# Kernel optimization log

Hardware: AMD Instinct MI355X
Metric: run time of the kernel (lower is better)

## Reference

```python
import jax, jax.numpy as jnp
import numpy as np

WS = 7        # window_size
SHIFT = 3     # shift_size
NH = 3        # num_heads
E = 96        # embed_dim
B, H, W = 8, 224, 224


def _relative_position_index(ws: int) -> np.ndarray:
    coords = np.stack(np.meshgrid(np.arange(ws), np.arange(ws), indexing='ij')).reshape(2, -1)
    rel = coords[:, :, None] - coords[:, None, :]          # (2, N, N)
    rel = rel.transpose(1, 2, 0) + (ws - 1)                # (N, N, 2)
    rel[:, :, 0] *= 2 * ws - 1
    return rel.sum(-1)                                      # (N, N) in [0, (2ws-1)^2)


def setup_inputs() -> dict:
    key = jax.random.key(0)
    ks = jax.random.split(key, 6)
    x = jax.random.normal(ks[0], (B, H, W, E), dtype=jnp.float32)
    # nn.MultiheadAttention params: packed in_proj (3E,E)+(3E,), out_proj (E,E)+(E,)
    w_qkv = jax.random.normal(ks[1], (3 * E, E), dtype=jnp.float32) * 0.02
    b_qkv = jax.random.normal(ks[2], (3 * E,), dtype=jnp.float32) * 0.02
    w_out = jax.random.normal(ks[3], (E, E), dtype=jnp.float32) * 0.02
    b_out = jax.random.normal(ks[4], (E,), dtype=jnp.float32) * 0.02
    bias_table = jax.random.normal(ks[5], ((2 * WS - 1) ** 2, NH), dtype=jnp.float32) * 0.02
    rel_index = jnp.asarray(_relative_position_index(WS), dtype=jnp.int32)
    return {"x": x, "w_qkv": w_qkv, "b_qkv": b_qkv, "w_out": w_out,
            "b_out": b_out, "bias_table": bias_table, "rel_index": rel_index}


def reference(x, w_qkv, b_qkv, w_out, b_out, bias_table, rel_index):
    ws, shift = WS, SHIFT
    Bq, Hq, Wq, C = x.shape
    nh = bias_table.shape[-1]
    hd = C // nh
    N = ws * ws

    # cyclic shift
    xs = jnp.roll(x, (-shift, -shift), axis=(1, 2))

    Hp = -(-Hq // ws) * ws
    Wp = -(-Wq // ws) * ws
    xs = jnp.pad(xs, ((0, 0), (0, Hp - Hq), (0, Wp - Wq), (0, 0)))

    # window partition -> (B*nW, N, C)
    win = xs.reshape(Bq, Hp // ws, ws, Wp // ws, ws, C)
    win = win.transpose(0, 1, 3, 2, 4, 5).reshape(-1, N, C)

    # packed QKV projection (torch Linear: x @ W.T + b)
    qkv = win @ w_qkv.T + b_qkv
    q, k, v = jnp.split(qkv, 3, axis=-1)
    hsplit = lambda t: t.reshape(t.shape[0], N, nh, hd)
    q, k, v = hsplit(q), hsplit(k), hsplit(v)

    # scaled attention scores + relative position bias (used as attn_mask in torch)
    scale = 1.0 / jnp.sqrt(jnp.asarray(hd, dtype=q.dtype))
    scores = jnp.einsum('bnhd,bmhd->bhnm', q * scale, k)    # (B*nW, h, N, N)
    bias = bias_table[rel_index].transpose(2, 0, 1)         # (h, N, N)
    attn = jax.nn.softmax(scores + bias[None], axis=-1)

    out = jnp.einsum('bhnm,bmhd->bnhd', attn, v).reshape(-1, N, C)
    out = out @ w_out.T + b_out

    # window reverse + crop + reverse shift
    out = out.reshape(Bq, Hp // ws, Wp // ws, ws, ws, C)
    out = out.transpose(0, 1, 3, 2, 4, 5).reshape(Bq, Hp, Wp, C)[:, :Hq, :Wq, :]
    return jnp.roll(out, (shift, shift), axis=(1, 2))
```

## Files before the change

kernel.cpp:

```cpp
#include <hip/hip_runtime.h>
#include <cstddef>


typedef _Float16 half8 __attribute__((ext_vector_type(8)));
typedef float f4v __attribute__((ext_vector_type(4)));
typedef unsigned short u16;
typedef unsigned int u32;

#define MFMA(A, B, C) __builtin_amdgcn_mfma_f32_16x16x32_f16((A), (B), (C), 0, 0, 0)

__device__ inline u16 f16b(float f) { return __builtin_bit_cast(u16, (_Float16)f); }
__device__ inline u32 pkrtz(float a, float b) {
    return __builtin_bit_cast(u32, __builtin_amdgcn_cvt_pkrtz(a, b));
}
__device__ inline int SWU(int a, int kg) {
    return (((a ^ (kg << 1) ^ ((a & 8) >> 1)) & 15) | (kg << 4));
}

__global__ void prep_kernel(const float* __restrict__ wqkv, const float* __restrict__ wout,
                            const float* __restrict__ btab, const int* __restrict__ ridx,
                            const float* __restrict__ bqkv,
                            u16* __restrict__ wq16, u16* __restrict__ wo16,
                            float* __restrict__ bmf, float* __restrict__ bqs)
{
    const int i = blockIdx.x * 256 + threadIdx.x;
    const float LOG2E = 1.4426950408889634f;
    const float QS = 0.17677669529663688f * LOG2E;
    if (i < 27648) {
        float f = wqkv[i];
        if (i < 9216) f *= QS;
        wq16[i] = f16b(f);
    } else if (i < 36864) {
        wo16[i - 27648] = f16b(wout[i - 27648]);
    } else if (i < 49152) {
        const int j  = i - 36864;
        const int fi = j & 3, ln = (j >> 2) & 63, fw = (j >> 8) & 3;
        const int fut = (j >> 10) & 3, fh = j >> 12;
        const int u  = fut * 16 + (ln >> 4) * 4 + fi;
        const int tt = fw * 16 + (ln & 15);
        float v;
        if (u >= 49)      v = -1e30f;
        else if (tt >= 49) v = 0.f;
        else               v = btab[ridx[tt * 49 + u] * 3 + fh] * LOG2E;
        bmf[j] = v;
    } else if (i < 49440) {
        const int j = i - 49152;
        float f = bqkv[j];
        if (j < 96) f *= QS;
        bqs[j] = f;
    }
}

__global__ __launch_bounds__(256, 4)
void swin_kernel(const float* __restrict__ x,
                 const u16* __restrict__ wq16,
                 const u16* __restrict__ wo16,
                 const float* __restrict__ bqs,
                 const float* __restrict__ bout,
                 const float* __restrict__ bmf,
                 float* __restrict__ out)
{
    __shared__ __attribute__((aligned(16))) char smem[40960];
    constexpr int QT = 0, KT = 12288, VT = 24576, PL = 36864;

    const int tid  = threadIdx.x;
    const int w    = tid >> 6;
    const int lane = tid & 63;
    const int l15  = lane & 15;
    const int lg   = lane >> 4;

    const int blk = blockIdx.x;
    const int bb  = blk >> 10;
    const int wi7 = ((blk >> 5) & 31) * 7;
    const int wj7 = (blk & 31) * 7;

    const int swbase = SWU(l15, lg) * 16;
    const int elb    = ((lg & 1) * 4) * 2;

    half8 xb[4][3];
    #pragma unroll
    for (int m = 0; m < 4; ++m) {
        const int t = m * 16 + l15;
        const int tr = t / 7, tc = t - tr * 7;
        int r = wi7 + tr + 3; if (r >= 224) r -= 224;
        int c = wj7 + tc + 3; if (c >= 224) c -= 224;
        const float* xrow = x + ((size_t)((bb * 224 + r) * 224 + c)) * 96 + lg * 8;
        #pragma unroll
        for (int ks = 0; ks < 3; ++ks) {
            const float4 f0 = *(const float4*)(xrow + ks * 32);
            const float4 f1 = *(const float4*)(xrow + ks * 32 + 4);
            uint4 pk;
            pk.x = pkrtz(f0.x, f0.y); pk.y = pkrtz(f0.z, f0.w);
            pk.z = pkrtz(f1.x, f1.y); pk.w = pkrtz(f1.z, f1.w);
            xb[m][ks] = __builtin_bit_cast(half8, pk);
        }
    }
    {
        const u16* wbase = wq16 + (size_t)l15 * 96 + lg * 8;
        half8 bcur[3], bnxt[3];
        int n = w;
        {
            const u16* p = wbase + n * 1536;
            bcur[0] = *(const half8*)(p);
            bcur[1] = *(const half8*)(p + 32);
            bcur[2] = *(const half8*)(p + 64);
        }
        while (true) {
            const int n2 = n + 4;
            if (n2 < 18) {
                const u16* p = wbase + n2 * 1536;
                bnxt[0] = *(const half8*)(p);
                bnxt[1] = *(const half8*)(p + 32);
                bnxt[2] = *(const half8*)(p + 64);
            }
            if (n < 12) {
                const float4 b4 = *(const float4*)(bqs + n * 16 + lg * 4);
                const int kg = ((n & 1) << 1) + (lg >> 1);
                const int fr0 = (n < 6) ? (QT + (((n >> 1) * 4) << 10))
                                        : (KT + ((((n - 6) >> 1) * 4) << 10));
                #pragma unroll
                for (int m = 0; m < 4; ++m) {
                    f4v acc = {0.f, 0.f, 0.f, 0.f};
                    acc = MFMA(bcur[0], xb[m][0], acc);
                    acc = MFMA(bcur[1], xb[m][1], acc);
                    acc = MFMA(bcur[2], xb[m][2], acc);
                    uint2 pv;
                    pv.x = pkrtz(acc[0] + b4.x, acc[1] + b4.y);
                    pv.y = pkrtz(acc[2] + b4.z, acc[3] + b4.w);
                    *(uint2*)(smem + fr0 + (m << 10) + SWU(l15, kg) * 16 + elb) = pv;
                }
            } else {
                const float bv = bqs[n * 16 + l15];
                const int hh = (n - 12) >> 1, nd = n & 1;
                const int fr0 = VT + (((hh * 2 + nd) * 2) << 10);
                #pragma unroll
                for (int m = 0; m < 4; ++m) {
                    f4v acc = {0.f, 0.f, 0.f, 0.f};
                    acc = MFMA(xb[m][0], bcur[0], acc);
                    acc = MFMA(xb[m][1], bcur[1], acc);
                    acc = MFMA(xb[m][2], bcur[2], acc);
                    uint2 pv;
                    pv.x = pkrtz(acc[0] + bv, acc[1] + bv);
                    pv.y = pkrtz(acc[2] + bv, acc[3] + bv);
                    const int kg = ((m & 1) << 1) + (lg >> 1);
                    *(uint2*)(smem + fr0 + ((m >> 1) << 10) + SWU(l15, kg) * 16 + elb) = pv;
                }
            }
            if (n2 >= 18) break;
            bcur[0] = bnxt[0]; bcur[1] = bnxt[1]; bcur[2] = bnxt[2];
            n = n2;
        }
    }
    __syncthreads();

    {
        const int plb = PL + (w << 10);
        half8 qaC, qaN;
        half8 kb[2][4];
        f4v   s[2][4];
        f4v   bC[4];

        qaC = *(const half8*)(smem + QT + ((0 * 4 + w) << 10) + swbase);
        #pragma unroll
        for (int ut = 0; ut < 4; ++ut)
            kb[0][ut] = *(const half8*)(smem + KT + ((0 * 4 + ut) << 10) + swbase);
        {
            const float* bb0 = bmf + w * 256 + lane * 4;
            #pragma unroll
            for (int ut = 0; ut < 4; ++ut) bC[ut] = *(const f4v*)(bb0 + ut * 1024);
        }
        #pragma unroll
        for (int ut = 0; ut < 4; ++ut)
            s[0][ut] = MFMA(kb[0][ut], qaC, bC[ut]);

        #pragma unroll
        for (int h = 0; h < 3; ++h) {
            const int cur = h & 1, nxt = cur ^ 1;
            const int qfr = QT + ((h * 4 + w) << 10);
            if (h < 2) {
                qaN = *(const half8*)(smem + QT + (((h + 1) * 4 + w) << 10) + swbase);
                #pragma unroll
                for (int ut = 0; ut < 4; ++ut)
                    kb[nxt][ut] = *(const half8*)(smem + KT + (((h + 1) * 4 + ut) << 10) + swbase);
                const float* bbn = bmf + (h + 1) * 4096 + w * 256 + lane * 4;
                #pragma unroll
                for (int ut = 0; ut < 4; ++ut) bC[ut] = *(const f4v*)(bbn + ut * 1024);
            }
            float mx = fmaxf(fmaxf(s[cur][0][0], s[cur][0][1]), fmaxf(s[cur][0][2], s[cur][0][3]));
            #pragma unroll
            for (int ut = 1; ut < 4; ++ut) {
                mx = fmaxf(mx, fmaxf(fmaxf(s[cur][ut][0], s[cur][ut][1]),
                                     fmaxf(s[cur][ut][2], s[cur][ut][3])));
            }
            mx = fmaxf(mx, __shfl_xor(mx, 16));
            mx = fmaxf(mx, __shfl_xor(mx, 32));
            float sm = 0.f;
            #pragma unroll
            for (int ut = 0; ut < 4; ++ut)
                #pragma unroll
                for (int i = 0; i < 4; ++i) {
                    const float e = exp2f(s[cur][ut][i] - mx);
                    s[cur][ut][i] = e; sm += e;
                }
            sm += __shfl_xor(sm, 16);
            sm += __shfl_xor(sm, 32);
            const float inv = 1.f / sm;
            #pragma unroll
            for (int ut = 0; ut < 4; ++ut) {
                uint2 pv;
                pv.x = pkrtz(s[cur][ut][0] * inv, s[cur][ut][1] * inv);
                pv.y = pkrtz(s[cur][ut][2] * inv, s[cur][ut][3] * inv);
                const int kg = (ut & 1) * 2 + (lg >> 1);
                const int base = (ut < 2) ? qfr : plb;
                *(uint2*)(smem + base + SWU(l15, kg) * 16 + elb) = pv;
            }
            const half8 vb00 = *(const half8*)(smem + VT + (((h * 2 + 0) * 2 + 0) << 10) + swbase);
            const half8 vb01 = *(const half8*)(smem + VT + (((h * 2 + 0) * 2 + 1) << 10) + swbase);
            const half8 vb10 = *(const half8*)(smem + VT + (((h * 2 + 1) * 2 + 0) << 10) + swbase);
            const half8 vb11 = *(const half8*)(smem + VT + (((h * 2 + 1) * 2 + 1) << 10) + swbase);
            if (h < 2) {
                #pragma unroll
                for (int ut = 0; ut < 4; ++ut)
                    s[nxt][ut] = MFMA(kb[nxt][ut], qaN, bC[ut]);
            }
            const half8 p0 = *(const half8*)(smem + qfr + swbase);
            const half8 p1 = *(const half8*)(smem + plb + swbase);
            #pragma unroll
            for (int nd = 0; nd < 2; ++nd) {
                f4v o = {0.f, 0.f, 0.f, 0.f};
                o = MFMA(nd ? vb10 : vb00, p0, o);
                o = MFMA(nd ? vb11 : vb01, p1, o);
                uint2 ov;
                ov.x = pkrtz(o[0], o[1]);
                ov.y = pkrtz(o[2], o[3]);
                *(uint2*)(smem + qfr + SWU(l15, nd * 2 + (lg >> 1)) * 16 + elb) = ov;
            }
        }
    }

    {
        const half8 ob0 = *(const half8*)(smem + QT + ((0 * 4 + w) << 10) + swbase);
        const half8 ob1 = *(const half8*)(smem + QT + ((1 * 4 + w) << 10) + swbase);
        const half8 ob2 = *(const half8*)(smem + QT + ((2 * 4 + w) << 10) + swbase);
        const int t = w * 16 + l15;
        float* obase = nullptr;
        if (t < 49) {
            const int tr = t / 7, tc = t - tr * 7;
            int r = wi7 + tr + 3; if (r >= 224) r -= 224;
            int c = wj7 + tc + 3; if (c >= 224) c -= 224;
            obase = out + ((size_t)((bb * 224 + r) * 224 + c)) * 96;
        }
        #pragma unroll
        for (int nn = 0; nn < 6; ++nn) {
            const u16* wp = wo16 + (size_t)(nn * 16 + l15) * 96 + lg * 8;
            f4v acc = {0.f, 0.f, 0.f, 0.f};
            acc = MFMA(*(const half8*)(wp),      ob0, acc);
            acc = MFMA(*(const half8*)(wp + 32), ob1, acc);
            acc = MFMA(*(const half8*)(wp + 64), ob2, acc);
            if (obase) {
                const float4 bo = *(const float4*)(bout + nn * 16 + lg * 4);
                float4 res;
                res.x = acc[0] + bo.x; res.y = acc[1] + bo.y;
                res.z = acc[2] + bo.z; res.w = acc[3] + bo.w;
                *(float4*)(obase + nn * 16 + lg * 4) = res;
            }
        }
    }
}

extern "C" void kernel_launch(void* const* d_in, const int* in_sizes, int n_in,
                              void* d_out, int out_size, void* d_ws, size_t ws_size,
                              hipStream_t stream) {
    const float* x          = (const float*)d_in[0];
    const float* w_qkv      = (const float*)d_in[1];
    const float* b_qkv      = (const float*)d_in[2];
    const float* w_out      = (const float*)d_in[3];
    const float* b_out      = (const float*)d_in[4];
    const float* bias_table = (const float*)d_in[5];
    const int*   rel_index  = (const int*)d_in[6];
    float* outp = (float*)d_out;

    u16* wq16 = (u16*)d_ws;
    u16* wo16 = wq16 + 27648;
    float* bmf = (float*)((char*)d_ws + 73728);
    float* bqs = (float*)((char*)d_ws + 122880);

    prep_kernel<<<dim3(194), dim3(256), 0, stream>>>(
        w_qkv, w_out, bias_table, rel_index, b_qkv, wq16, wo16, bmf, bqs);
    swin_kernel<<<dim3(8192), dim3(256), 0, stream>>>(
        x, wq16, wo16, bqs, b_out, bmf, outp);
}
```

Measured before the change: 208.7 us.

## Keep Q and attention output in registers via bpermute, shrink LDS for occupancy

Each wave now computes the Q projection for only its own 16 tokens and keeps the result in registers. A ds_bpermute reshuffle turns it into the MFMA operand layout, so the Q tile never goes through LDS. The attention output is regathered the same way and feeds the output projection straight from registers. LDS shrinks from 40 KB to 32 KB and launch bounds go from 4 to 5 blocks per CU, aiming at higher occupancy. The cost is more cross-lane permute work, the loss of the software pipelining of the next head's score MFMA, and possible register pressure under the tighter bound.

```diff
diff --git a/kernel.cpp b/kernel.cpp
--- a/kernel.cpp
+++ b/kernel.cpp
@@ -8,6 +8,7 @@
 typedef unsigned int u32;
 
 #define MFMA(A, B, C) __builtin_amdgcn_mfma_f32_16x16x32_f16((A), (B), (C), 0, 0, 0)
+#define BPERM(addr, val) __builtin_amdgcn_ds_bpermute((addr), (val))
 
 __device__ inline u16 f16b(float f) { return __builtin_bit_cast(u16, (_Float16)f); }
 __device__ inline u32 pkrtz(float a, float b) {
@@ -39,7 +40,7 @@
         const int u  = fut * 16 + (ln >> 4) * 4 + fi;
         const int tt = fw * 16 + (ln & 15);
         float v;
-        if (u >= 49)      v = -1e30f;
+        if (u >= 49)       v = -1e30f;
         else if (tt >= 49) v = 0.f;
         else               v = btab[ridx[tt * 49 + u] * 3 + fh] * LOG2E;
         bmf[j] = v;
@@ -51,7 +52,7 @@
     }
 }
 
-__global__ __launch_bounds__(256, 4)
+__global__ __launch_bounds__(256, 5)
 void swin_kernel(const float* __restrict__ x,
                  const u16* __restrict__ wq16,
                  const u16* __restrict__ wo16,
@@ -60,8 +61,8 @@
                  const float* __restrict__ bmf,
                  float* __restrict__ out)
 {
-    __shared__ __attribute__((aligned(16))) char smem[40960];
-    constexpr int QT = 0, KT = 12288, VT = 24576, PL = 36864;
+    __shared__ __attribute__((aligned(16))) char smem[32768];
+    constexpr int KT = 0, VT = 12288, PP = 24576;
 
     const int tid  = threadIdx.x;
     const int w    = tid >> 6;
@@ -75,16 +76,16 @@
     const int wj7 = (blk & 31) * 7;
 
     const int swbase = SWU(l15, lg) * 16;
-    const int elb    = ((lg & 1) * 4) * 2;
-
-    half8 xb[4][3];
-    #pragma unroll
-    for (int m = 0; m < 4; ++m) {
-        const int t = m * 16 + l15;
+    const int elb    = (lg & 1) * 8;
+
+    auto pixoff = [&](int t) -> size_t {
         const int tr = t / 7, tc = t - tr * 7;
         int r = wi7 + tr + 3; if (r >= 224) r -= 224;
         int c = wj7 + tc + 3; if (c >= 224) c -= 224;
-        const float* xrow = x + ((size_t)((bb * 224 + r) * 224 + c)) * 96 + lg * 8;
+        return ((size_t)((bb * 224 + r) * 224 + c)) * 96;
+    };
+    auto loadxb = [&](int t, half8* dst) {
+        const float* xrow = x + pixoff(t) + lg * 8;
         #pragma unroll
         for (int ks = 0; ks < 3; ++ks) {
             const float4 f0 = *(const float4*)(xrow + ks * 32);
@@ -92,106 +93,136 @@
             uint4 pk;
             pk.x = pkrtz(f0.x, f0.y); pk.y = pkrtz(f0.z, f0.w);
             pk.z = pkrtz(f1.x, f1.y); pk.w = pkrtz(f1.z, f1.w);
-            xb[m][ks] = __builtin_bit_cast(half8, pk);
-        }
-    }
+            dst[ks] = __builtin_bit_cast(half8, pk);
+        }
+    };
+
+    u32 qd[12];
     {
+        half8 xbw[3];
+        loadxb(w * 16 + l15, xbw);
         const u16* wbase = wq16 + (size_t)l15 * 96 + lg * 8;
         half8 bcur[3], bnxt[3];
-        int n = w;
-        {
-            const u16* p = wbase + n * 1536;
-            bcur[0] = *(const half8*)(p);
-            bcur[1] = *(const half8*)(p + 32);
-            bcur[2] = *(const half8*)(p + 64);
-        }
-        while (true) {
-            const int n2 = n + 4;
-            if (n2 < 18) {
-                const u16* p = wbase + n2 * 1536;
+        bcur[0] = *(const half8*)(wbase);
+        bcur[1] = *(const half8*)(wbase + 32);
+        bcur[2] = *(const half8*)(wbase + 64);
+        #pragma unroll
+        for (int n = 0; n < 6; ++n) {
+            if (n < 5) {
+                const u16* p = wbase + (n + 1) * 1536;
                 bnxt[0] = *(const half8*)(p);
                 bnxt[1] = *(const half8*)(p + 32);
                 bnxt[2] = *(const half8*)(p + 64);
             }
-            if (n < 12) {
-                const float4 b4 = *(const float4*)(bqs + n * 16 + lg * 4);
-                const int kg = ((n & 1) << 1) + (lg >> 1);
-                const int fr0 = (n < 6) ? (QT + (((n >> 1) * 4) << 10))
-                                        : (KT + ((((n - 6) >> 1) * 4) << 10));
-                #pragma unroll
-                for (int m = 0; m < 4; ++m) {
+            f4v acc = {0.f, 0.f, 0.f, 0.f};
+            acc = MFMA(bcur[0], xbw[0], acc);
+            acc = MFMA(bcur[1], xbw[1], acc);
+            acc = MFMA(bcur[2], xbw[2], acc);
+            const float4 b4 = *(const float4*)(bqs + n * 16 + lg * 4);
+            qd[2 * n]     = pkrtz(acc[0] + b4.x, acc[1] + b4.y);
+            qd[2 * n + 1] = pkrtz(acc[2] + b4.z, acc[3] + b4.w);
+            if (n < 5) { bcur[0] = bnxt[0]; bcur[1] = bnxt[1]; bcur[2] = bnxt[2]; }
+        }
+    }
+
+    {
+        half8 kvw[3][3];
+        #pragma unroll
+        for (int i = 0; i < 3; ++i) {
+            const u16* p = wq16 + (size_t)(6 + w + 4 * i) * 1536 + (size_t)l15 * 96 + lg * 8;
+            kvw[i][0] = *(const half8*)(p);
+            kvw[i][1] = *(const half8*)(p + 32);
+            kvw[i][2] = *(const half8*)(p + 64);
+        }
+        half8 xc[3], xn[3];
+        loadxb(l15, xc);
+        #pragma unroll
+        for (int m = 0; m < 4; ++m) {
+            if (m < 3) loadxb((m + 1) * 16 + l15, xn);
+            #pragma unroll
+            for (int i = 0; i < 3; ++i) {
+                const int n = 6 + w + 4 * i;
+                if (n < 12) {
                     f4v acc = {0.f, 0.f, 0.f, 0.f};
-                    acc = MFMA(bcur[0], xb[m][0], acc);
-                    acc = MFMA(bcur[1], xb[m][1], acc);
-                    acc = MFMA(bcur[2], xb[m][2], acc);
+                    acc = MFMA(kvw[i][0], xc[0], acc);
+                    acc = MFMA(kvw[i][1], xc[1], acc);
+                    acc = MFMA(kvw[i][2], xc[2], acc);
+                    const float4 b4 = *(const float4*)(bqs + n * 16 + lg * 4);
                     uint2 pv;
                     pv.x = pkrtz(acc[0] + b4.x, acc[1] + b4.y);
                     pv.y = pkrtz(acc[2] + b4.z, acc[3] + b4.w);
+                    const int kg  = ((n & 1) << 1) + (lg >> 1);
+                    const int fr0 = KT + ((((n - 6) >> 1) * 4) << 10);
                     *(uint2*)(smem + fr0 + (m << 10) + SWU(l15, kg) * 16 + elb) = pv;
-                }
-            } else {
-                const float bv = bqs[n * 16 + l15];
-                const int hh = (n - 12) >> 1, nd = n & 1;
-                const int fr0 = VT + (((hh * 2 + nd) * 2) << 10);
-                #pragma unroll
-                for (int m = 0; m < 4; ++m) {
+                } else {
                     f4v acc = {0.f, 0.f, 0.f, 0.f};
-                    acc = MFMA(xb[m][0], bcur[0], acc);
-                    acc = MFMA(xb[m][1], bcur[1], acc);
-                    acc = MFMA(xb[m][2], bcur[2], acc);
+                    acc = MFMA(xc[0], kvw[i][0], acc);
+                    acc = MFMA(xc[1], kvw[i][1], acc);
+                    acc = MFMA(xc[2], kvw[i][2], acc);
+                    const float bv = bqs[n * 16 + l15];
                     uint2 pv;
                     pv.x = pkrtz(acc[0] + bv, acc[1] + bv);
                     pv.y = pkrtz(acc[2] + bv, acc[3] + bv);
+                    const int hh = (n - 12) >> 1, nd = n & 1;
                     const int kg = ((m & 1) << 1) + (lg >> 1);
-                    *(uint2*)(smem + fr0 + ((m >> 1) << 10) + SWU(l15, kg) * 16 + elb) = pv;
+                    *(uint2*)(smem + VT + ((((hh * 2 + nd) * 2) + (m >> 1)) << 10) +
+                              SWU(l15, kg) * 16 + elb) = pv;
                 }
             }
-            if (n2 >= 18) break;
-            bcur[0] = bnxt[0]; bcur[1] = bnxt[1]; bcur[2] = bnxt[2];
-            n = n2;
-        }
+            if (m < 3) { xc[0] = xn[0]; xc[1] = xn[1]; xc[2] = xn[2]; }
+        }
+    }
+
+    const int sl0 = (l15 + 16 * ((lg & 1) * 2)) << 2;
+    const int sl1 = sl0 + (16 << 2);
+    const bool hi = (lg >= 2);
+    half8 qa[3];
+    #pragma unroll
+    for (int h = 0; h < 3; ++h) {
+        const int A0 = BPERM(sl0, (int)qd[4 * h + 0]), B0 = BPERM(sl0, (int)qd[4 * h + 2]);
+        const int A1 = BPERM(sl0, (int)qd[4 * h + 1]), B1 = BPERM(sl0, (int)qd[4 * h + 3]);
+        const int A2 = BPERM(sl1, (int)qd[4 * h + 0]), B2 = BPERM(sl1, (int)qd[4 * h + 2]);
+        const int A3 = BPERM(sl1, (int)qd[4 * h + 1]), B3 = BPERM(sl1, (int)qd[4 * h + 3]);
+        uint4 qw;
+        qw.x = (u32)(hi ? B0 : A0);
+        qw.y = (u32)(hi ? B1 : A1);
+        qw.z = (u32)(hi ? B2 : A2);
+        qw.w = (u32)(hi ? B3 : A3);
+        qa[h] = __builtin_bit_cast(half8, qw);
     }
     __syncthreads();
 
+    uint4 obw[3];
     {
-        const int plb = PL + (w << 10);
-        half8 qaC, qaN;
-        half8 kb[2][4];
-        f4v   s[2][4];
-        f4v   bC[4];
-
-        qaC = *(const half8*)(smem + QT + ((0 * 4 + w) << 10) + swbase);
+        const int ppb = PP + (w << 11);
+        half8 kb[4]; f4v bC[4];
         #pragma unroll
         for (int ut = 0; ut < 4; ++ut)
-            kb[0][ut] = *(const half8*)(smem + KT + ((0 * 4 + ut) << 10) + swbase);
+            kb[ut] = *(const half8*)(smem + KT + (ut << 10) + swbase);
         {
-            const float* bb0 = bmf + w * 256 + lane * 4;
-            #pragma unroll
-            for (int ut = 0; ut < 4; ++ut) bC[ut] = *(const f4v*)(bb0 + ut * 1024);
-        }
-        #pragma unroll
-        for (int ut = 0; ut < 4; ++ut)
-            s[0][ut] = MFMA(kb[0][ut], qaC, bC[ut]);
-
+            const float* bp = bmf + w * 256 + lane * 4;
+            #pragma unroll
+            for (int ut = 0; ut < 4; ++ut) bC[ut] = *(const f4v*)(bp + ut * 1024);
+        }
         #pragma unroll
         for (int h = 0; h < 3; ++h) {
-            const int cur = h & 1, nxt = cur ^ 1;
-            const int qfr = QT + ((h * 4 + w) << 10);
+            f4v s[4];
+            #pragma unroll
+            for (int ut = 0; ut < 4; ++ut)
+                s[ut] = MFMA(kb[ut], qa[h], bC[ut]);
             if (h < 2) {
-                qaN = *(const half8*)(smem + QT + (((h + 1) * 4 + w) << 10) + swbase);
                 #pragma unroll
                 for (int ut = 0; ut < 4; ++ut)
-                    kb[nxt][ut] = *(const half8*)(smem + KT + (((h + 1) * 4 + ut) << 10) + swbase);
-                const float* bbn = bmf + (h + 1) * 4096 + w * 256 + lane * 4;
+                    kb[ut] = *(const half8*)(smem + KT + (((h + 1) * 4 + ut) << 10) + swbase);
+                const float* bp = bmf + (h + 1) * 4096 + w * 256 + lane * 4;
                 #pragma unroll
-                for (int ut = 0; ut < 4; ++ut) bC[ut] = *(const f4v*)(bbn + ut * 1024);
-            }
-            float mx = fmaxf(fmaxf(s[cur][0][0], s[cur][0][1]), fmaxf(s[cur][0][2], s[cur][0][3]));
-            #pragma unroll
-            for (int ut = 1; ut < 4; ++ut) {
-                mx = fmaxf(mx, fmaxf(fmaxf(s[cur][ut][0], s[cur][ut][1]),
-                                     fmaxf(s[cur][ut][2], s[cur][ut][3])));
-            }
+                for (int ut = 0; ut < 4; ++ut) bC[ut] = *(const f4v*)(bp + ut * 1024);
+            }
+            float mx = -1e30f;
+            #pragma unroll
+            for (int ut = 0; ut < 4; ++ut)
+                #pragma unroll
+                for (int i = 0; i < 4; ++i) mx = fmaxf(mx, s[ut][i]);
             mx = fmaxf(mx, __shfl_xor(mx, 16));
             mx = fmaxf(mx, __shfl_xor(mx, 32));
             float sm = 0.f;
@@ -199,8 +230,8 @@
             for (int ut = 0; ut < 4; ++ut)
                 #pragma unroll
                 for (int i = 0; i < 4; ++i) {
-                    const float e = exp2f(s[cur][ut][i] - mx);
-                    s[cur][ut][i] = e; sm += e;
+                    const float e = exp2f(s[ut][i] - mx);
+                    s[ut][i] = e; sm += e;
                 }
             sm += __shfl_xor(sm, 16);
             sm += __shfl_xor(sm, 32);
@@ -208,48 +239,47 @@
             #pragma unroll
             for (int ut = 0; ut < 4; ++ut) {
                 uint2 pv;
-                pv.x = pkrtz(s[cur][ut][0] * inv, s[cur][ut][1] * inv);
-                pv.y = pkrtz(s[cur][ut][2] * inv, s[cur][ut][3] * inv);
+                pv.x = pkrtz(s[ut][0] * inv, s[ut][1] * inv);
+                pv.y = pkrtz(s[ut][2] * inv, s[ut][3] * inv);
                 const int kg = (ut & 1) * 2 + (lg >> 1);
-                const int base = (ut < 2) ? qfr : plb;
+                const int base = (ut < 2) ? ppb : (ppb + 1024);
                 *(uint2*)(smem + base + SWU(l15, kg) * 16 + elb) = pv;
             }
             const half8 vb00 = *(const half8*)(smem + VT + (((h * 2 + 0) * 2 + 0) << 10) + swbase);
             const half8 vb01 = *(const half8*)(smem + VT + (((h * 2 + 0) * 2 + 1) << 10) + swbase);
             const half8 vb10 = *(const half8*)(smem + VT + (((h * 2 + 1) * 2 + 0) << 10) + swbase);
             const half8 vb11 = *(const half8*)(smem + VT + (((h * 2 + 1) * 2 + 1) << 10) + swbase);
-            if (h < 2) {
-                #pragma unroll
-                for (int ut = 0; ut < 4; ++ut)
-                    s[nxt][ut] = MFMA(kb[nxt][ut], qaN, bC[ut]);
-            }
-            const half8 p0 = *(const half8*)(smem + qfr + swbase);
-            const half8 p1 = *(const half8*)(smem + plb + swbase);
+            const half8 p0 = *(const half8*)(smem + ppb + swbase);
+            const half8 p1 = *(const half8*)(smem + ppb + 1024 + swbase);
+            u32 aw[4];
             #pragma unroll
             for (int nd = 0; nd < 2; ++nd) {
                 f4v o = {0.f, 0.f, 0.f, 0.f};
                 o = MFMA(nd ? vb10 : vb00, p0, o);
                 o = MFMA(nd ? vb11 : vb01, p1, o);
-                uint2 ov;
-                ov.x = pkrtz(o[0], o[1]);
-                ov.y = pkrtz(o[2], o[3]);
-                *(uint2*)(smem + qfr + SWU(l15, nd * 2 + (lg >> 1)) * 16 + elb) = ov;
+                aw[nd * 2]     = pkrtz(o[0], o[1]);
+                aw[nd * 2 + 1] = pkrtz(o[2], o[3]);
+            }
+            {
+                const int A0 = BPERM(sl0, (int)aw[0]), B0 = BPERM(sl0, (int)aw[2]);
+                const int A1 = BPERM(sl0, (int)aw[1]), B1 = BPERM(sl0, (int)aw[3]);
+                const int A2 = BPERM(sl1, (int)aw[0]), B2 = BPERM(sl1, (int)aw[2]);
+                const int A3 = BPERM(sl1, (int)aw[1]), B3 = BPERM(sl1, (int)aw[3]);
+                obw[h].x = (u32)(hi ? B0 : A0);
+                obw[h].y = (u32)(hi ? B1 : A1);
+                obw[h].z = (u32)(hi ? B2 : A2);
+                obw[h].w = (u32)(hi ? B3 : A3);
             }
         }
     }
 
     {
-        const half8 ob0 = *(const half8*)(smem + QT + ((0 * 4 + w) << 10) + swbase);
-        const half8 ob1 = *(const half8*)(smem + QT + ((1 * 4 + w) << 10) + swbase);
-        const half8 ob2 = *(const half8*)(smem + QT + ((2 * 4 + w) << 10) + swbase);
+        const half8 ob0 = __builtin_bit_cast(half8, obw[0]);
+        const half8 ob1 = __builtin_bit_cast(half8, obw[1]);
+        const half8 ob2 = __builtin_bit_cast(half8, obw[2]);
         const int t = w * 16 + l15;
         float* obase = nullptr;
-        if (t < 49) {
-            const int tr = t / 7, tc = t - tr * 7;
-            int r = wi7 + tr + 3; if (r >= 224) r -= 224;
-            int c = wj7 + tc + 3; if (c >= 224) c -= 224;
-            obase = out + ((size_t)((bb * 224 + r) * 224 + c)) * 96;
-        }
+        if (t < 49) obase = out + pixoff(t);
         #pragma unroll
         for (int nn = 0; nn < 6; ++nn) {
             const u16* wp = wo16 + (size_t)(nn * 16 + l15) * 96 + lg * 8;
```

Measured after the change: 468.0 us. 2.24x slower.
